# Performance work log

Measured on AMD Instinct MI355X. Metric: run time of the kernel, lower is better.

Reference implementation:

```python
import jax, jax.numpy as jnp
import numpy as np

NUM_LEVELS = 4
CODES_PER_LEVEL = 1024
CODE_DIM = 256
BATCH = 65536


def setup_inputs() -> dict:
    key = jax.random.key(0)
    k_z, k_cb = jax.random.split(key)
    z = jax.random.normal(k_z, (BATCH, CODE_DIM), dtype=jnp.float32)
    # codebooks buffer: randn * code_dim**-0.5, matching torch init
    codebooks = jax.random.normal(k_cb, (NUM_LEVELS, CODES_PER_LEVEL, CODE_DIM), dtype=jnp.float32) * (CODE_DIM ** -0.5)
    return {"z": z, "codebooks": codebooks}


def _quantize(z, codebooks):
    """Sequential residual VQ: per level, squared-dist argmin + gather.
    z: [B, D]; codebooks: [L, K, D]. Returns z_q [B, D], codes [B, L] int32.
    """
    residual = z
    z_q = jnp.zeros_like(z)
    codes_list = []
    for lvl in range(codebooks.shape[0]):  # small fixed loop over levels
        cb = codebooks[lvl]  # [K, D]
        # ||r - c||^2 = ||r||^2 - 2 r.c + ||c||^2  -> [B, K]
        dists = (jnp.sum(residual * residual, axis=-1, keepdims=True)
                 - 2.0 * jnp.einsum('bd,kd->bk', residual, cb)
                 + jnp.sum(cb * cb, axis=-1))
        codes_lvl = jnp.argmin(dists, axis=1)  # [B]
        selected = cb[codes_lvl]               # gather [B, D]
        z_q = z_q + selected
        residual = residual - selected
        codes_list.append(codes_lvl)
    codes = jnp.stack(codes_list, axis=1)  # [B, L]
    return z_q, codes


def reference(z, codebooks):
    z_q, codes = _quantize(z, codebooks)
    # straight-through: gradient flows to z only
    z_q_st = z + jax.lax.stop_gradient(z_q - z)
    commit_loss = jnp.mean(jnp.square(jax.lax.stop_gradient(z_q) - z))
    return z_q_st, codes, commit_loss
```

## Files before the change

kernel.cpp:

```cpp
#include <hip/hip_runtime.h>


#define NB 65536
#define ND 256
#define NK 1024
#define NL 4
#define MROWS 128
#define NBLK (NB / MROWS)
#define CHUNK 64
#define NCH (NK / CHUNK)
#define BSTR 264
#define FLAG_MARGIN 1e-3f

typedef __attribute__((ext_vector_type(8))) short short8;
typedef __attribute__((ext_vector_type(4))) float f32x4;

__device__ inline unsigned short f2bf(float x) {
  unsigned u = __float_as_uint(x);
  u = u + 0x7FFFu + ((u >> 16) & 1u);
  return (unsigned short)(u >> 16);
}
__device__ inline float bf2f(unsigned short h) {
  return __uint_as_float(((unsigned)h) << 16);
}

__device__ float np_sum256_sq(const float* __restrict__ a) {
#pragma clang fp contract(off)
  float out[2];
  for (int h = 0; h < 2; ++h) {
    const float* p = a + 128 * h;
    float r[8];
    for (int j = 0; j < 8; ++j) r[j] = p[j] * p[j];
    for (int i = 8; i < 128; i += 8)
      for (int j = 0; j < 8; ++j) r[j] += p[i + j] * p[i + j];
    out[h] = ((r[0] + r[1]) + (r[2] + r[3])) + ((r[4] + r[5]) + (r[6] + r[7]));
  }
  return out[0] + out[1];
}
__device__ float np_einsum256(const float* __restrict__ r,
                              const float* __restrict__ c) {
#pragma clang fp contract(off)
  float e[4] = {0.f, 0.f, 0.f, 0.f};
  for (int d = 0; d < 256; d += 4) {
    e[0] += r[d + 0] * c[d + 0];
    e[1] += r[d + 1] * c[d + 1];
    e[2] += r[d + 2] * c[d + 2];
    e[3] += r[d + 3] * c[d + 3];
  }
  return (e[0] + e[1]) + (e[2] + e[3]);
}
__device__ float np_dist(const float* __restrict__ resrow,
                         const float* __restrict__ crow, float r2) {
#pragma clang fp contract(off)
  float E = np_einsum256(resrow, crow);
  float c2 = np_sum256_sq(crow);
  float t1 = r2 - 2.0f * E;
  return t1 + c2;
}

__global__ void prep_split(const float* __restrict__ cb,
                           unsigned short* __restrict__ whi,
                           unsigned short* __restrict__ wlo) {
  int i = blockIdx.x * 256 + threadIdx.x;
  float c = cb[i];
  unsigned short h = f2bf(c);
  whi[i] = h;
  wlo[i] = f2bf(c - bf2f(h));
}
__global__ void prep_c2(const float* __restrict__ cb, float* __restrict__ c2) {
  int k = blockIdx.x;
  int lane = threadIdx.x;
  const float* p = cb + (size_t)k * ND + lane * 4;
  double s = (double)p[0]*p[0] + (double)p[1]*p[1]
           + (double)p[2]*p[2] + (double)p[3]*p[3];
  for (int off = 32; off >= 1; off >>= 1) s += __shfl_down(s, off);
  if (lane == 0) c2[k] = (float)s;
}


__global__ __launch_bounds__(256, 2)
void rvq_main(const float* __restrict__ z, const float* __restrict__ cbf,
              const unsigned short* __restrict__ whi,
              const unsigned short* __restrict__ wlo,
              const float* __restrict__ c2w, float* __restrict__ out) {
  extern __shared__ char smem[];
  unsigned short* bhi = (unsigned short*)smem;
  unsigned short* blo = bhi + 64 * BSTR;
  float* c2s  = (float*)(smem + 67584);
  int*   selh = (int*)(smem + 71680);
  int*   flags= (int*)(smem + 73728);
  float* mscr = (float*)smem;
  float* resr = (float*)(smem + 32768);
  float* redf = (float*)(smem + 34816);
  int*   redk = (int*)(smem + 35840);
  double* lred= (double*)smem;

  const int tid  = threadIdx.x;
  const int wave = tid >> 6, lane = tid & 63;
  const int quad = lane >> 4, lx = lane & 15;
  const int blk  = blockIdx.x;

  for (int lvl = 0; lvl < NL; ++lvl) {
    __syncthreads();
#pragma unroll
    for (int t = 0; t < 4; ++t)
      c2s[t * 256 + tid] = c2w[lvl * NK + t * 256 + tid];

    short8 Ah[2][8], Al[2][8];
#pragma unroll
    for (int s = 0; s < 2; ++s) {
      const int rloc = wave * 32 + s * 16 + lx;
      const size_t rg = (size_t)(blk * MROWS + rloc);
#pragma unroll
      for (int ks = 0; ks < 8; ++ks) {
        const int k0 = 32 * ks + quad * 8;
        const float* zp = z + rg * ND + k0;
        float4 p0 = *(const float4*)zp;
        float4 p1 = *(const float4*)(zp + 4);
        for (int l = 0; l < lvl; ++l) {
          int sel = selh[rloc * 4 + l];
          const float* cp = cbf + (size_t)(l * NK + sel) * ND + k0;
          float4 q0 = *(const float4*)cp, q1 = *(const float4*)(cp + 4);
          p0.x -= q0.x; p0.y -= q0.y; p0.z -= q0.z; p0.w -= q0.w;
          p1.x -= q1.x; p1.y -= q1.y; p1.z -= q1.z; p1.w -= q1.w;
        }
        float v0[8] = {p0.x, p0.y, p0.z, p0.w, p1.x, p1.y, p1.z, p1.w};
#pragma unroll
        for (int j = 0; j < 8; ++j) {
          unsigned short h = f2bf(v0[j]);
          Ah[s][ks][j] = (short)h;
          Al[s][ks][j] = (short)f2bf(v0[j] - bf2f(h));
        }
      }
    }

    float m1[8], m2[8]; int i1[8];
#pragma unroll
    for (int t = 0; t < 8; ++t) { m1[t] = 1e30f; m2[t] = 1e30f; i1[t] = 0; }

#pragma unroll 1
    for (int ch = 0; ch < NCH; ++ch) {
      __syncthreads();
      {
        const size_t gb = (size_t)lvl * NK * ND + (size_t)ch * CHUNK * ND;
#pragma unroll
        for (int it = 0; it < 8; ++it) {
          int i = it * 256 + tid;
          int code = i >> 5, col = i & 31;
          uint4 vh = *(const uint4*)(whi + gb + (size_t)code * ND + col * 8);
          *(uint4*)(bhi + code * BSTR + col * 8) = vh;
          uint4 vl = *(const uint4*)(wlo + gb + (size_t)code * ND + col * 8);
          *(uint4*)(blo + code * BSTR + col * 8) = vl;
        }
      }
      __syncthreads();
#pragma unroll 1
      for (int tile = 0; tile < 4; ++tile) {
        f32x4 a0a = {0,0,0,0}, a0b = {0,0,0,0}, a1a = {0,0,0,0}, a1b = {0,0,0,0};
        const int crow = tile * 16 + lx;
        const unsigned short* bph = bhi + crow * BSTR + quad * 8;
        const unsigned short* bpl = blo + crow * BSTR + quad * 8;
#pragma unroll
        for (int ks = 0; ks < 8; ks += 2) {
          short8 vb0 = *(const short8*)(bph + 32 * ks);
          short8 wb0 = *(const short8*)(bpl + 32 * ks);
          short8 vb1 = *(const short8*)(bph + 32 * ks + 32);
          short8 wb1 = *(const short8*)(bpl + 32 * ks + 32);
          a0a = __builtin_amdgcn_mfma_f32_16x16x32_bf16(Ah[0][ks], vb0, a0a, 0, 0, 0);
          a1a = __builtin_amdgcn_mfma_f32_16x16x32_bf16(Ah[1][ks], vb0, a1a, 0, 0, 0);
          a0a = __builtin_amdgcn_mfma_f32_16x16x32_bf16(Al[0][ks], vb0, a0a, 0, 0, 0);
          a1a = __builtin_amdgcn_mfma_f32_16x16x32_bf16(Al[1][ks], vb0, a1a, 0, 0, 0);
          a0a = __builtin_amdgcn_mfma_f32_16x16x32_bf16(Ah[0][ks], wb0, a0a, 0, 0, 0);
          a1a = __builtin_amdgcn_mfma_f32_16x16x32_bf16(Ah[1][ks], wb0, a1a, 0, 0, 0);
          a0b = __builtin_amdgcn_mfma_f32_16x16x32_bf16(Ah[0][ks + 1], vb1, a0b, 0, 0, 0);
          a1b = __builtin_amdgcn_mfma_f32_16x16x32_bf16(Ah[1][ks + 1], vb1, a1b, 0, 0, 0);
          a0b = __builtin_amdgcn_mfma_f32_16x16x32_bf16(Al[0][ks + 1], vb1, a0b, 0, 0, 0);
          a1b = __builtin_amdgcn_mfma_f32_16x16x32_bf16(Al[1][ks + 1], vb1, a1b, 0, 0, 0);
          a0b = __builtin_amdgcn_mfma_f32_16x16x32_bf16(Ah[0][ks + 1], wb1, a0b, 0, 0, 0);
          a1b = __builtin_amdgcn_mfma_f32_16x16x32_bf16(Ah[1][ks + 1], wb1, a1b, 0, 0, 0);
        }
        const int kidx = ch * CHUNK + crow;
        const float c2v = c2s[kidx];
#pragma unroll
        for (int s = 0; s < 2; ++s)
#pragma unroll
          for (int r = 0; r < 4; ++r) {
            float e = (s == 0) ? (a0a[r] + a0b[r]) : (a1a[r] + a1b[r]);
            float d = fmaf(-2.0f, e, c2v);
            int st = s * 4 + r;
            if (d < m1[st]) { m2[st] = m1[st]; m1[st] = d; i1[st] = kidx; }
            else if (d < m2[st]) m2[st] = d;
          }
      }
    }

    __syncthreads();
#pragma unroll
    for (int t = 0; t < 8; ++t) {
      int rloc = wave * 32 + (t >> 2) * 16 + quad * 4 + (t & 3);
      float* p = mscr + (rloc * 16 + lx) * 4;
      p[0] = m1[t]; p[1] = m2[t]; p[2] = __int_as_float(i1[t]);
    }
    __syncthreads();
    if (tid < MROWS) {
      float gm1 = 1e30f, gm2 = 1e30f; int gi1 = 0x7fffffff;
      for (int t = 0; t < 16; ++t) {
        const float* p = mscr + (tid * 16 + t) * 4;
        float a1 = p[0], a2 = p[1]; int ai = __float_as_int(p[2]);
        if (a1 < gm1 || (a1 == gm1 && ai < gi1)) {
          gm2 = fminf(gm1, a2); gm1 = a1; gi1 = ai;
        } else {
          gm2 = fminf(gm2, a1);
        }
      }
      selh[tid * 4 + lvl] = gi1;
      flags[tid] = (gm2 - gm1 <= FLAG_MARGIN) ? 1 : 0;
    }
    __syncthreads();

    for (int r = 0; r < MROWS; ++r) {
      if (flags[r]) {
        {
          float v = z[(size_t)(blk * MROWS + r) * ND + tid];
          for (int l = 0; l < lvl; ++l)
            v -= cbf[(size_t)(l * NK + selh[r * 4 + l]) * ND + tid];
          resr[tid] = v;
        }
        __syncthreads();
        float r2 = np_sum256_sq(resr);
        float bd = 1e30f; int bk = 0x7fffffff;
        for (int u = 0; u < 4; ++u) {
          int k = u * 256 + tid;
          float dd = np_dist(resr, cbf + (size_t)(lvl * NK + k) * ND, r2);
          if (dd < bd || (dd == bd && k < bk)) { bd = dd; bk = k; }
        }
        redf[tid] = bd; redk[tid] = bk;
        __syncthreads();
        if (tid == 0) {
          float gb = 1e30f; int gk = 0x7fffffff;
          for (int t2 = 0; t2 < 256; ++t2) {
            if (redf[t2] < gb || (redf[t2] == gb && redk[t2] < gk)) {
              gb = redf[t2]; gk = redk[t2];
            }
          }
          selh[r * 4 + lvl] = gk;
        }
        __syncthreads();
      }
    }
  }

  __syncthreads();
  double lacc = 0.0;
#pragma unroll 1
  for (int it = 0; it < 32; ++it) {
    int i = it * 256 + tid;
    int row = i >> 6, dc = i & 63;
    size_t rg = (size_t)(blk * MROWS + row);
    float4 z4 = *(const float4*)(z + rg * ND + dc * 4);
    float4 q; q.x = 0.f; q.y = 0.f; q.z = 0.f; q.w = 0.f;
    for (int l = 0; l < NL; ++l) {
      int sel = selh[row * 4 + l];
      float4 c4 = *(const float4*)(cbf + (size_t)(l * NK + sel) * ND + dc * 4);
      q.x += c4.x; q.y += c4.y; q.z += c4.z; q.w += c4.w;
    }
    *(float4*)(out + rg * ND + dc * 4) = q;
    float dx = q.x - z4.x, dy = q.y - z4.y, dz = q.z - z4.z, dw = q.w - z4.w;
    lacc += (double)dx * dx + (double)dy * dy + (double)dz * dz + (double)dw * dw;
  }
  if (tid < MROWS) {
    for (int l = 0; l < NL; ++l)
      out[(size_t)NB * ND + (size_t)(blk * MROWS + tid) * NL + l] =
          (float)selh[tid * 4 + l];
  }
  __syncthreads();
  lred[tid] = lacc;
  __syncthreads();
  if (tid == 0) {
    double s = 0.0;
    for (int t = 0; t < 256; ++t) s += lred[t];
    atomicAdd(out + (size_t)NB * ND + (size_t)NB * NL,
              (float)(s / ((double)NB * (double)ND)));
  }
}

extern "C" void kernel_launch(void* const* d_in, const int* in_sizes, int n_in,
                              void* d_out, int out_size, void* d_ws, size_t ws_size,
                              hipStream_t stream) {
  const float* z  = (const float*)d_in[0];
  const float* cb = (const float*)d_in[1];
  float* out = (float*)d_out;

  unsigned short* whi = (unsigned short*)d_ws;
  unsigned short* wlo = whi + (size_t)NL * NK * ND;
  float* c2w = (float*)(wlo + (size_t)NL * NK * ND);

  hipMemsetAsync((void*)(out + (size_t)NB * ND + (size_t)NB * NL), 0,
                 sizeof(float), stream);

  prep_split<<<dim3(4096), dim3(256), 0, stream>>>(cb, whi, wlo);
  prep_c2<<<dim3(4096), dim3(64), 0, stream>>>(cb, c2w);

  const size_t shmem = 74240;
  hipFuncSetAttribute((const void*)rvq_main,
                      hipFuncAttributeMaxDynamicSharedMemorySize, (int)shmem);
  rvq_main<<<dim3(NBLK), dim3(256), shmem, stream>>>(z, cb, whi, wlo, c2w, out);
}
```

Measured before the change: 1.213 ms.

## Replace split-bf16 triple MFMA with single fp16 MFMA and pre-swizzled codebook blobs

```diff
diff --git a/kernel.cpp b/kernel.cpp
--- a/kernel.cpp
+++ b/kernel.cpp
@@ -7,22 +7,14 @@
 #define NL 4
 #define MROWS 128
 #define NBLK (NB / MROWS)
-#define CHUNK 64
-#define NCH (NK / CHUNK)
-#define BSTR 264
-#define FLAG_MARGIN 1e-3f
-
-typedef __attribute__((ext_vector_type(8))) short short8;
+#define NCH 16
+#define FLAG_MARGIN 1.2e-2f
+
+typedef _Float16 half8_t __attribute__((ext_vector_type(8)));
+typedef __fp16 fp16x2 __attribute__((ext_vector_type(2)));
 typedef __attribute__((ext_vector_type(4))) float f32x4;
 
-__device__ inline unsigned short f2bf(float x) {
-  unsigned u = __float_as_uint(x);
-  u = u + 0x7FFFu + ((u >> 16) & 1u);
-  return (unsigned short)(u >> 16);
-}
-__device__ inline float bf2f(unsigned short h) {
-  return __uint_as_float(((unsigned)h) << 16);
-}
+union h8u { half8_t v; fp16x2 h2[4]; uint4 u; };
 
 __device__ float np_sum256_sq(const float* __restrict__ a) {
 #pragma clang fp contract(off)
@@ -58,14 +50,22 @@
   return t1 + c2;
 }
 
-__global__ void prep_split(const float* __restrict__ cb,
-                           unsigned short* __restrict__ whi,
-                           unsigned short* __restrict__ wlo) {
-  int i = blockIdx.x * 256 + threadIdx.x;
-  float c = cb[i];
-  unsigned short h = f2bf(c);
-  whi[i] = h;
-  wlo[i] = f2bf(c - bf2f(h));
+__global__ void prep_blob(const float* __restrict__ cb,
+                          unsigned short* __restrict__ wfp) {
+  int U = blockIdx.x * 256 + threadIdx.x;
+  int lane = U & 63, blob = U >> 6;
+  int s = blob & 7, t = (blob >> 3) & 3, ch = (blob >> 5) & 15, lvl = blob >> 9;
+  int code = ch * 64 + t * 16 + (lane & 15);
+  int k0 = s * 32 + (lane >> 4) * 8;
+  const float* p = cb + (size_t)(lvl * NK + code) * ND + k0;
+  float4 x0 = *(const float4*)p;
+  float4 x1 = *(const float4*)(p + 4);
+  h8u u;
+  u.h2[0] = __builtin_amdgcn_cvt_pkrtz(x0.x, x0.y);
+  u.h2[1] = __builtin_amdgcn_cvt_pkrtz(x0.z, x0.w);
+  u.h2[2] = __builtin_amdgcn_cvt_pkrtz(x1.x, x1.y);
+  u.h2[3] = __builtin_amdgcn_cvt_pkrtz(x1.z, x1.w);
+  ((uint4*)wfp)[U] = u.u;
 }
 __global__ void prep_c2(const float* __restrict__ cb, float* __restrict__ c2) {
   int k = blockIdx.x;
@@ -78,22 +78,20 @@
 }
 
 
-__global__ __launch_bounds__(256, 2)
+__global__ __launch_bounds__(256, 4)
 void rvq_main(const float* __restrict__ z, const float* __restrict__ cbf,
-              const unsigned short* __restrict__ whi,
-              const unsigned short* __restrict__ wlo,
+              const unsigned short* __restrict__ wfp,
               const float* __restrict__ c2w, float* __restrict__ out) {
   extern __shared__ char smem[];
-  unsigned short* bhi = (unsigned short*)smem;
-  unsigned short* blo = bhi + 64 * BSTR;
-  float* c2s  = (float*)(smem + 67584);
-  int*   selh = (int*)(smem + 71680);
-  int*   flags= (int*)(smem + 73728);
+  half8_t* bblob = (half8_t*)smem;
+  float* c2s  = (float*)(smem + 32768);
+  int*   selh = (int*)(smem + 36864);
+  int*   flags= (int*)(smem + 38912);
   float* mscr = (float*)smem;
+  double* lred= (double*)smem;
   float* resr = (float*)(smem + 32768);
-  float* redf = (float*)(smem + 34816);
-  int*   redk = (int*)(smem + 35840);
-  double* lred= (double*)smem;
+  float* redf = (float*)(smem + 33792);
+  int*   redk = (int*)(smem + 34816);
 
   const int tid  = threadIdx.x;
   const int wave = tid >> 6, lane = tid & 63;
@@ -106,31 +104,31 @@
     for (int t = 0; t < 4; ++t)
       c2s[t * 256 + tid] = c2w[lvl * NK + t * 256 + tid];
 
-    short8 Ah[2][8], Al[2][8];
+    half8_t A[2][8];
 #pragma unroll
     for (int s = 0; s < 2; ++s) {
       const int rloc = wave * 32 + s * 16 + lx;
       const size_t rg = (size_t)(blk * MROWS + rloc);
+      const float* cbase[NL];
+      for (int l = 0; l < lvl; ++l)
+        cbase[l] = cbf + (size_t)(l * NK + selh[rloc * 4 + l]) * ND;
 #pragma unroll
       for (int ks = 0; ks < 8; ++ks) {
-        const int k0 = 32 * ks + quad * 8;
-        const float* zp = z + rg * ND + k0;
-        float4 p0 = *(const float4*)zp;
-        float4 p1 = *(const float4*)(zp + 4);
+        const int k0 = ks * 32 + quad * 8;
+        float4 p0 = *(const float4*)(z + rg * ND + k0);
+        float4 p1 = *(const float4*)(z + rg * ND + k0 + 4);
         for (int l = 0; l < lvl; ++l) {
-          int sel = selh[rloc * 4 + l];
-          const float* cp = cbf + (size_t)(l * NK + sel) * ND + k0;
-          float4 q0 = *(const float4*)cp, q1 = *(const float4*)(cp + 4);
+          float4 q0 = *(const float4*)(cbase[l] + k0);
+          float4 q1 = *(const float4*)(cbase[l] + k0 + 4);
           p0.x -= q0.x; p0.y -= q0.y; p0.z -= q0.z; p0.w -= q0.w;
           p1.x -= q1.x; p1.y -= q1.y; p1.z -= q1.z; p1.w -= q1.w;
         }
-        float v0[8] = {p0.x, p0.y, p0.z, p0.w, p1.x, p1.y, p1.z, p1.w};
-#pragma unroll
-        for (int j = 0; j < 8; ++j) {
-          unsigned short h = f2bf(v0[j]);
-          Ah[s][ks][j] = (short)h;
-          Al[s][ks][j] = (short)f2bf(v0[j] - bf2f(h));
-        }
+        h8u u;
+        u.h2[0] = __builtin_amdgcn_cvt_pkrtz(p0.x, p0.y);
+        u.h2[1] = __builtin_amdgcn_cvt_pkrtz(p0.z, p0.w);
+        u.h2[2] = __builtin_amdgcn_cvt_pkrtz(p1.x, p1.y);
+        u.h2[3] = __builtin_amdgcn_cvt_pkrtz(p1.z, p1.w);
+        A[s][ks] = u.v;
       }
     }
 
@@ -142,55 +140,33 @@
     for (int ch = 0; ch < NCH; ++ch) {
       __syncthreads();
       {
-        const size_t gb = (size_t)lvl * NK * ND + (size_t)ch * CHUNK * ND;
-#pragma unroll
-        for (int it = 0; it < 8; ++it) {
-          int i = it * 256 + tid;
-          int code = i >> 5, col = i & 31;
-          uint4 vh = *(const uint4*)(whi + gb + (size_t)code * ND + col * 8);
-          *(uint4*)(bhi + code * BSTR + col * 8) = vh;
-          uint4 vl = *(const uint4*)(wlo + gb + (size_t)code * ND + col * 8);
-          *(uint4*)(blo + code * BSTR + col * 8) = vl;
-        }
+        const uint4* src = (const uint4*)wfp + (size_t)(lvl * 16 + ch) * 2048;
+        uint4* dst = (uint4*)smem;
+#pragma unroll
+        for (int i = 0; i < 8; ++i)
+          dst[i * 256 + tid] = src[i * 256 + tid];
       }
       __syncthreads();
+
 #pragma unroll 1
-      for (int tile = 0; tile < 4; ++tile) {
-        f32x4 a0a = {0,0,0,0}, a0b = {0,0,0,0}, a1a = {0,0,0,0}, a1b = {0,0,0,0};
-        const int crow = tile * 16 + lx;
-        const unsigned short* bph = bhi + crow * BSTR + quad * 8;
-        const unsigned short* bpl = blo + crow * BSTR + quad * 8;
-#pragma unroll
-        for (int ks = 0; ks < 8; ks += 2) {
-          short8 vb0 = *(const short8*)(bph + 32 * ks);
-          short8 wb0 = *(const short8*)(bpl + 32 * ks);
-          short8 vb1 = *(const short8*)(bph + 32 * ks + 32);
-          short8 wb1 = *(const short8*)(bpl + 32 * ks + 32);
-          a0a = __builtin_amdgcn_mfma_f32_16x16x32_bf16(Ah[0][ks], vb0, a0a, 0, 0, 0);
-          a1a = __builtin_amdgcn_mfma_f32_16x16x32_bf16(Ah[1][ks], vb0, a1a, 0, 0, 0);
-          a0a = __builtin_amdgcn_mfma_f32_16x16x32_bf16(Al[0][ks], vb0, a0a, 0, 0, 0);
-          a1a = __builtin_amdgcn_mfma_f32_16x16x32_bf16(Al[1][ks], vb0, a1a, 0, 0, 0);
-          a0a = __builtin_amdgcn_mfma_f32_16x16x32_bf16(Ah[0][ks], wb0, a0a, 0, 0, 0);
-          a1a = __builtin_amdgcn_mfma_f32_16x16x32_bf16(Ah[1][ks], wb0, a1a, 0, 0, 0);
-          a0b = __builtin_amdgcn_mfma_f32_16x16x32_bf16(Ah[0][ks + 1], vb1, a0b, 0, 0, 0);
-          a1b = __builtin_amdgcn_mfma_f32_16x16x32_bf16(Ah[1][ks + 1], vb1, a1b, 0, 0, 0);
-          a0b = __builtin_amdgcn_mfma_f32_16x16x32_bf16(Al[0][ks + 1], vb1, a0b, 0, 0, 0);
-          a1b = __builtin_amdgcn_mfma_f32_16x16x32_bf16(Al[1][ks + 1], vb1, a1b, 0, 0, 0);
-          a0b = __builtin_amdgcn_mfma_f32_16x16x32_bf16(Ah[0][ks + 1], wb1, a0b, 0, 0, 0);
-          a1b = __builtin_amdgcn_mfma_f32_16x16x32_bf16(Ah[1][ks + 1], wb1, a1b, 0, 0, 0);
-        }
-        const int kidx = ch * CHUNK + crow;
+      for (int t4 = 0; t4 < 4; ++t4) {
+        f32x4 a0 = {0.f, 0.f, 0.f, 0.f}, a1 = {0.f, 0.f, 0.f, 0.f};
+        const half8_t* bb = bblob + t4 * 512 + lane;
+#pragma unroll
+        for (int s = 0; s < 8; ++s) {
+          half8_t bv = bb[s * 64];
+          a0 = __builtin_amdgcn_mfma_f32_16x16x32_f16(A[0][s], bv, a0, 0, 0, 0);
+          a1 = __builtin_amdgcn_mfma_f32_16x16x32_f16(A[1][s], bv, a1, 0, 0, 0);
+        }
+        const int kidx = ch * 64 + t4 * 16 + lx;
         const float c2v = c2s[kidx];
 #pragma unroll
-        for (int s = 0; s < 2; ++s)
-#pragma unroll
-          for (int r = 0; r < 4; ++r) {
-            float e = (s == 0) ? (a0a[r] + a0b[r]) : (a1a[r] + a1b[r]);
-            float d = fmaf(-2.0f, e, c2v);
-            int st = s * 4 + r;
-            if (d < m1[st]) { m2[st] = m1[st]; m1[st] = d; i1[st] = kidx; }
-            else if (d < m2[st]) m2[st] = d;
-          }
+        for (int st = 0; st < 8; ++st) {
+          float e = (st < 4) ? a0[st & 3] : a1[st & 3];
+          float d = fmaf(-2.0f, e, c2v);
+          if (d < m1[st]) { m2[st] = m1[st]; m1[st] = d; i1[st] = kidx; }
+          else if (d < m2[st]) m2[st] = d;
+        }
       }
     }
 
@@ -206,11 +182,11 @@
       float gm1 = 1e30f, gm2 = 1e30f; int gi1 = 0x7fffffff;
       for (int t = 0; t < 16; ++t) {
         const float* p = mscr + (tid * 16 + t) * 4;
-        float a1 = p[0], a2 = p[1]; int ai = __float_as_int(p[2]);
-        if (a1 < gm1 || (a1 == gm1 && ai < gi1)) {
-          gm2 = fminf(gm1, a2); gm1 = a1; gi1 = ai;
+        float a1v = p[0], a2v = p[1]; int ai = __float_as_int(p[2]);
+        if (a1v < gm1 || (a1v == gm1 && ai < gi1)) {
+          gm2 = fminf(gm1, a2v); gm1 = a1v; gi1 = ai;
         } else {
-          gm2 = fminf(gm2, a1);
+          gm2 = fminf(gm2, a1v);
         }
       }
       selh[tid * 4 + lvl] = gi1;
@@ -291,18 +267,15 @@
   const float* cb = (const float*)d_in[1];
   float* out = (float*)d_out;
 
-  unsigned short* whi = (unsigned short*)d_ws;
-  unsigned short* wlo = whi + (size_t)NL * NK * ND;
-  float* c2w = (float*)(wlo + (size_t)NL * NK * ND);
-
-  hipMemsetAsync((void*)(out + (size_t)NB * ND + (size_t)NB * NL), 0,
-                 sizeof(float), stream);
-
-  prep_split<<<dim3(4096), dim3(256), 0, stream>>>(cb, whi, wlo);
-  prep_c2<<<dim3(4096), dim3(64), 0, stream>>>(cb, c2w);
-
-  const size_t shmem = 74240;
-  hipFuncSetAttribute((const void*)rvq_main,
-                      hipFuncAttributeMaxDynamicSharedMemorySize, (int)shmem);
-  rvq_main<<<dim3(NBLK), dim3(256), shmem, stream>>>(z, cb, whi, wlo, c2w, out);
-}
+  unsigned short* wfp = (unsigned short*)d_ws;
+  float* c2w = (float*)(wfp + (size_t)NL * NK * ND);
+
+  (void)hipMemsetAsync((void*)(out + (size_t)NB * ND + (size_t)NB * NL), 0,
+                       sizeof(float), stream);
+
+  prep_blob<<<dim3(512), dim3(256), 0, stream>>>(cb, wfp);
+  prep_c2<<<dim3(NL * NK), dim3(64), 0, stream>>>(cb, c2w);
+
+  const size_t shmem = 39424;
+  rvq_main<<<dim3(NBLK), dim3(256), shmem, stream>>>(z, cb, wfp, c2w, out);
+}
```

After: 3.003 ms. +147.5%, slower.
